# Performance work log

Measured on AMD Instinct MI355X. Metric: run time of the kernel, lower is better.

The kernel has to match this reference:

```python
import jax, jax.numpy as jnp
import numpy as np

BETA = 0.25      # commitment loss weight
DECAY = 0.99     # EMA decay
EPS = 1e-5       # Laplace smoothing for counts


def setup_inputs() -> dict:
    key = jax.random.key(0)
    k1, k2, k3 = jax.random.split(key, 3)
    B, d, h, w, K = 16, 64, 64, 64, 1024
    z_e = jax.random.normal(k1, (B, d, h, w), dtype=jnp.float32)
    codebook = jax.random.normal(k2, (K, d), dtype=jnp.float32)
    ema_count = jnp.ones((K,), dtype=jnp.float32)
    ema_sum = jax.random.normal(k3, (K, d), dtype=jnp.float32)
    return {"z_e": z_e, "codebook": codebook, "ema_count": ema_count, "ema_sum": ema_sum}


def reference(z_e, codebook, ema_count, ema_sum):
    B, d, h, w = z_e.shape
    K = codebook.shape[0]
    # [B,d,h,w] -> [N,d], N = B*h*w
    z_flat = jnp.transpose(z_e, (0, 2, 3, 1)).reshape(-1, d)
    # squared euclidean distances [N,K]
    dist = (jnp.sum(z_flat * z_flat, axis=1, keepdims=True)
            - 2.0 * (z_flat @ codebook.T)
            + jnp.sum(codebook * codebook, axis=1)[None, :])
    indices = jnp.argmin(dist, axis=1)                      # [N] int
    e_k = codebook[indices].reshape(B, h, w, d).transpose(0, 3, 1, 2)  # [B,d,h,w]

    # --- EMA codebook update (training mode, no grad) ---
    zf = jax.lax.stop_gradient(z_flat)
    counts = jax.ops.segment_sum(jnp.ones((zf.shape[0],), dtype=zf.dtype), indices, num_segments=K)
    sums = jax.ops.segment_sum(zf, indices, num_segments=K)
    new_count = ema_count * DECAY + (1.0 - DECAY) * counts
    new_sum = ema_sum * DECAY + (1.0 - DECAY) * sums
    n = jnp.sum(new_count)
    count_s = (new_count + EPS) / (n + K * EPS) * n
    new_codebook = new_sum / count_s[:, None]

    # straight-through estimator
    e_k_ste = z_e + jax.lax.stop_gradient(e_k - z_e)
    L_commit = (jnp.mean((z_e - jax.lax.stop_gradient(e_k)) ** 2)
                + BETA * jnp.mean((jax.lax.stop_gradient(z_e) - e_k) ** 2))
    return (e_k_ste, indices.reshape(B, h, w), L_commit, new_codebook, new_count, new_sum)
```

## Files before the change

kernel.cpp:

```cpp
#include <hip/hip_runtime.h>
#include <hip/hip_bf16.h>
#include <hip/hip_fp16.h>

#define NB 16
#define DD 64
#define HW 4096
#define NTOT 65536
#define KC 1024

#define O_EK   0
#define O_IDX  4194304
#define O_L    4259840
#define O_CB   4259841
#define O_CNT  4325377
#define O_SUM  4326401

#define WS_IDX    0
#define WS_LCPART 65536
#define WS_N      66048
#define WS_CNORM  66560
#define WS_PSUM   67584
#define WS_PCNT   329728
#define WS_FLGC   333824
#define WS_FLGL   334336
#define WS_CBH    399360
#define WS_CBL    432128

#define MARGIN 0.002f
#define MAXFLG 32

typedef _Float16 v8h __attribute__((ext_vector_type(8)));
typedef float    v4f __attribute__((ext_vector_type(4)));

__global__ __launch_bounds__(256) void k_pre(const float* __restrict__ cb,
                                             const float* __restrict__ ema_count,
                                             float* __restrict__ cnorm,
                                             float* __restrict__ n_ws,
                                             unsigned short* __restrict__ cbh,
                                             unsigned short* __restrict__ cbl) {
    const int t = threadIdx.x;
    const int w = (blockIdx.x * 256 + t) >> 6;
    const int l = t & 63;
    float s = 0.f;
    if (l < 16) {
        float4 v = *(const float4*)(cb + (size_t)w * DD + l * 4);
        s = v.x * v.x + v.y * v.y + v.z * v.z + v.w * v.w;
    }
#pragma unroll
    for (int m = 1; m <= 8; m <<= 1) s += __shfl_xor(s, m, 64);
    if (l == 0) cnorm[w] = s;

    const int e4 = blockIdx.x * 256 + t;
    if (e4 < 16384) {
        float4 v4 = ((const float4*)cb)[e4];
        __half hx = __float2half(v4.x), hy = __float2half(v4.y),
               hz = __float2half(v4.z), hw2 = __float2half(v4.w);
        ushort4 h4 = { __half_as_ushort(hx), __half_as_ushort(hy),
                       __half_as_ushort(hz), __half_as_ushort(hw2) };
        ((ushort4*)cbh)[e4] = h4;
        ushort4 l4 = { __half_as_ushort(__float2half(v4.x - __half2float(hx))),
                       __half_as_ushort(__float2half(v4.y - __half2float(hy))),
                       __half_as_ushort(__float2half(v4.z - __half2float(hz))),
                       __half_as_ushort(__float2half(v4.w - __half2float(hw2))) };
        ((ushort4*)cbl)[e4] = l4;
    }

    if (blockIdx.x == 0) {
        __shared__ float red[256];
        red[t] = ema_count[t] + ema_count[t + 256] + ema_count[t + 512] + ema_count[t + 768];
        __syncthreads();
        for (int s2 = 128; s2 >= 1; s2 >>= 1) {
            if (t < s2) red[t] += red[t + s2];
            __syncthreads();
        }
        if (t == 0) n_ws[0] = 0.99f * red[0] + 0.01f * 65536.0f;
    }
}

__global__ __launch_bounds__(256) void k_argmin(const float* __restrict__ z_e,
                                                const unsigned short* __restrict__ cbh,
                                                const unsigned short* __restrict__ cbl,
                                                const float* __restrict__ cnorm,
                                                int* __restrict__ idx_ws,
                                                int* __restrict__ flg_cnt,
                                                int* __restrict__ flg_list,
                                                float* __restrict__ out) {
    __shared__ __align__(16) unsigned short Ah[128 * 72];
    __shared__ __align__(16) unsigned short Al[128 * 72];
    __shared__ __align__(16) unsigned short Bs[2][128 * 72];
    __shared__ __align__(16) float cn_lds[KC];
    __shared__ float znl[128];
    __shared__ int   idx_lds[128];
    __shared__ int   flagrows[128];
    __shared__ int   nflag;

    unsigned short* Bh = &Bs[0][0];
    unsigned short* Bl = &Bs[1][0];
    float* Atf = (float*)&Bs[0][0];

    const int t  = threadIdx.x;
    const int n0 = blockIdx.x * 128;
    const int b   = n0 >> 12;
    const int hw0 = n0 & 4095;
    const float* zbase = z_e + (size_t)b * (DD * HW) + hw0;

    if (t == 0) nflag = 0;
    *(float4*)&cn_lds[t * 4] = *(const float4*)(cnorm + t * 4);

#pragma unroll
    for (int s = 0; s < 8; ++s) {
        int idx = t + s * 256;
        int j   = idx >> 5;
        int i4  = (idx & 31) << 2;
        float4 v = *(const float4*)(zbase + (size_t)j * HW + i4);
        *(float4*)(&Atf[j * 128 + i4]) = v;
    }
    __syncthreads();

    {
        const int m  = t & 127;
        const int j0 = (t >> 7) * 32;
#pragma unroll 4
        for (int jj = 0; jj < 32; jj += 2) {
            int j = j0 + jj;
            float v0 = Atf[j * 128 + m];
            float v1 = Atf[(j + 1) * 128 + m];
            __half h0 = __float2half(v0), h1 = __float2half(v1);
            __half l0 = __float2half(v0 - __half2float(h0));
            __half l1 = __float2half(v1 - __half2float(h1));
            *(unsigned*)&Ah[m * 72 + j] = (unsigned)__half_as_ushort(h0) | ((unsigned)__half_as_ushort(h1) << 16);
            *(unsigned*)&Al[m * 72 + j] = (unsigned)__half_as_ushort(l0) | ((unsigned)__half_as_ushort(l1) << 16);
        }
    }
    __syncthreads();

    if (t < 128) {
        float s = 0.f;
        for (int j = 0; j < 64; ++j) { float a = Atf[j * 128 + t]; s = fmaf(a, a, s); }
        znl[t] = s;
    }

    const int w    = t >> 6;
    const int lane = t & 63;
    const int c    = lane & 15;
    const int q    = lane >> 4;

    v8h Afh[2][2], Afl[2][2];
#pragma unroll
    for (int g = 0; g < 2; ++g) {
        int m = 32 * w + 16 * g + c;
#pragma unroll
        for (int s = 0; s < 2; ++s) {
            Afh[g][s] = *(const v8h*)&Ah[m * 72 + s * 32 + q * 8];
            Afl[g][s] = *(const v8h*)&Al[m * 72 + s * 32 + q * 8];
        }
    }

    float m1v[2][4], m2v[2][4]; int m1i[2][4];
#pragma unroll
    for (int g = 0; g < 2; ++g)
#pragma unroll
        for (int r = 0; r < 4; ++r) { m1v[g][r] = 3.4e38f; m2v[g][r] = 3.4e38f; m1i[g][r] = 0; }

    for (int kt = 0; kt < 8; ++kt) {
        __syncthreads();
#pragma unroll
        for (int s2 = 0; s2 < 4; ++s2) {
            int idx = t + s2 * 256;
            int code = idx >> 3;
            int off  = (idx & 7) * 8;
            size_t gsrc = ((size_t)(kt * 128 + code)) * 64 + off;
            *(uint4*)&Bh[code * 72 + off] = *(const uint4*)(cbh + gsrc);
            *(uint4*)&Bl[code * 72 + off] = *(const uint4*)(cbl + gsrc);
        }
        __syncthreads();

#pragma unroll
        for (int sub = 0; sub < 8; ++sub) {
            const int cl = sub * 16 + c;
            v8h Bfh0 = *(const v8h*)&Bh[cl * 72 + q * 8];
            v8h Bfh1 = *(const v8h*)&Bh[cl * 72 + 32 + q * 8];
            v8h Bfl0 = *(const v8h*)&Bl[cl * 72 + q * 8];
            v8h Bfl1 = *(const v8h*)&Bl[cl * 72 + 32 + q * 8];
            float cnc = cn_lds[kt * 128 + cl];
            const int kg = kt * 128 + cl;
#pragma unroll
            for (int g = 0; g < 2; ++g) {
                v4f acc = {0.f, 0.f, 0.f, 0.f};
                acc = __builtin_amdgcn_mfma_f32_16x16x32_f16(Afh[g][0], Bfh0, acc, 0, 0, 0);
                acc = __builtin_amdgcn_mfma_f32_16x16x32_f16(Afh[g][1], Bfh1, acc, 0, 0, 0);
                acc = __builtin_amdgcn_mfma_f32_16x16x32_f16(Afh[g][0], Bfl0, acc, 0, 0, 0);
                acc = __builtin_amdgcn_mfma_f32_16x16x32_f16(Afh[g][1], Bfl1, acc, 0, 0, 0);
                acc = __builtin_amdgcn_mfma_f32_16x16x32_f16(Afl[g][0], Bfh0, acc, 0, 0, 0);
                acc = __builtin_amdgcn_mfma_f32_16x16x32_f16(Afl[g][1], Bfh1, acc, 0, 0, 0);
#pragma unroll
                for (int r = 0; r < 4; ++r) {
                    float v = fmaf(-2.0f, acc[r], cnc);
                    bool better = v < m1v[g][r];
                    m2v[g][r] = better ? m1v[g][r] : fminf(m2v[g][r], v);
                    m1i[g][r] = better ? kg : m1i[g][r];
                    m1v[g][r] = better ? v : m1v[g][r];
                }
            }
        }
    }

#pragma unroll
    for (int g = 0; g < 2; ++g)
#pragma unroll
        for (int r = 0; r < 4; ++r) {
            float a = m1v[g][r], b2 = m2v[g][r]; int ii = m1i[g][r];
#pragma unroll
            for (int mask = 1; mask <= 8; mask <<= 1) {
                float ov = __shfl_xor(a, mask, 64);
                int   oi = __shfl_xor(ii, mask, 64);
                float o2 = __shfl_xor(b2, mask, 64);
                bool take = (ov < a) || (ov == a && oi < ii);
                float loser = take ? a : ov;
                b2 = fminf(fminf(b2, o2), loser);
                a  = take ? ov : a;
                ii = take ? oi : ii;
            }
            if (c == 0) {
                int row = 32 * w + 16 * g + q * 4 + r;
                idx_lds[row] = ii;
                if ((b2 - a) < MARGIN) { int p = atomicAdd(&nflag, 1); flagrows[p] = row; }
            }
        }
    __syncthreads();

    int nf = nflag; if (nf > MAXFLG) nf = MAXFLG;
    if (t == 0) flg_cnt[blockIdx.x] = nf;
    if (t < nf) flg_list[blockIdx.x * MAXFLG + t] = flagrows[t];

    if (t < 128) {
        int bi = idx_lds[t];
        out[O_IDX + n0 + t] = (float)bi;
        idx_ws[n0 + t] = bi;
    }
}

__global__ __launch_bounds__(256) void k_fix(const float* __restrict__ z_e,
                                             const float* __restrict__ cb,
                                             const float* __restrict__ cnorm,
                                             const int* __restrict__ flg_cnt,
                                             const int* __restrict__ flg_list,
                                             int* __restrict__ idx_ws,
                                             float* __restrict__ out) {
    const int blk = blockIdx.x;
    const int nf = flg_cnt[blk];
    if (nf == 0) return;
    __shared__ float redv4[4];
    __shared__ int   redi4[4];
    const int t = threadIdx.x;
    const int lane = t & 63, w = t >> 6;
    const int n0 = blk * 128;
    const int b   = n0 >> 12;
    const int hw0 = n0 & 4095;

    for (int f = 0; f < nf; ++f) {
        int row = flg_list[blk * MAXFLG + f];
        const float* zrow = z_e + (size_t)b * (DD * HW) + hw0 + row;
        float znr = 0.f;
        for (int j = 0; j < 64; ++j) { float v = zrow[(size_t)j * HW]; znr = fmaf(v, v, znr); }
        float best = 3.4e38f; int bi = 0;
#pragma unroll
        for (int c2 = 0; c2 < 4; ++c2) {
            int k = t * 4 + c2;
            const float* ck = cb + (size_t)k * DD;
            float acc = 0.f;
            for (int j = 0; j < 64; ++j) acc = fmaf(zrow[(size_t)j * HW], ck[j], acc);
            float v = (znr - 2.0f * acc) + cnorm[k];
            if (v < best) { best = v; bi = k; }
        }
#pragma unroll
        for (int mask = 1; mask <= 32; mask <<= 1) {
            float ov = __shfl_xor(best, mask, 64);
            int   oi = __shfl_xor(bi, mask, 64);
            if (ov < best || (ov == best && oi < bi)) { best = ov; bi = oi; }
        }
        if (lane == 0) { redv4[w] = best; redi4[w] = bi; }
        __syncthreads();
        if (t == 0) {
            float bv = redv4[0]; int bix = redi4[0];
#pragma unroll
            for (int w2 = 1; w2 < 4; ++w2)
                if (redv4[w2] < bv || (redv4[w2] == bv && redi4[w2] < bix)) { bv = redv4[w2]; bix = redi4[w2]; }
            idx_ws[n0 + row] = bix;
            out[O_IDX + n0 + row] = (float)bix;
        }
        __syncthreads();
    }
}

__global__ __launch_bounds__(1024) void k_out(const int* __restrict__ idx_ws,
                                              const float* __restrict__ z_e,
                                              const float* __restrict__ cb,
                                              float* __restrict__ psum,
                                              int* __restrict__ pcnt,
                                              float* __restrict__ lc_part,
                                              float* __restrict__ out) {
    __shared__ float acc[KC];
    __shared__ int bins[KC];
    __shared__ float cbj[KC];
    __shared__ float lcr[16];
    const int j = blockIdx.x & 63;
    const int c = blockIdx.x >> 6;
    const int t = threadIdx.x;
    acc[t] = 0.f;
    bins[t] = 0;
    cbj[t] = cb[(size_t)t * DD + j];
    __syncthreads();
    const float* zj = z_e + (size_t)j * HW;
    float* oj = out + O_EK + (size_t)j * HW;
    const int base = c * 16384;
    float lc = 0.f;
#pragma unroll
    for (int i = 0; i < 4; ++i) {
        int n4 = base + i * 4096 + t * 4;
        int b = n4 >> 12, hw = n4 & 4095;
        size_t zoff = (size_t)b * (DD * HW) + hw;
        float4 z4 = *(const float4*)(zj + zoff);
        int4   k4 = *(const int4*)(idx_ws + n4);
        float e0 = cbj[k4.x], e1 = cbj[k4.y], e2 = cbj[k4.z], e3 = cbj[k4.w];
        float4 o4 = { z4.x + (e0 - z4.x), z4.y + (e1 - z4.y),
                      z4.z + (e2 - z4.z), z4.w + (e3 - z4.w) };
        *(float4*)(oj + zoff) = o4;
        float d0 = z4.x - e0, d1 = z4.y - e1, d2 = z4.z - e2, d3 = z4.w - e3;
        lc = fmaf(d0, d0, lc); lc = fmaf(d1, d1, lc);
        lc = fmaf(d2, d2, lc); lc = fmaf(d3, d3, lc);
        atomicAdd(&acc[k4.x], z4.x);
        atomicAdd(&acc[k4.y], z4.y);
        atomicAdd(&acc[k4.z], z4.z);
        atomicAdd(&acc[k4.w], z4.w);
        if (j == 0) {
            atomicAdd(&bins[k4.x], 1); atomicAdd(&bins[k4.y], 1);
            atomicAdd(&bins[k4.z], 1); atomicAdd(&bins[k4.w], 1);
        }
    }
    __syncthreads();
    psum[(size_t)c * 65536 + j * 1024 + t] = acc[t];
    if (j == 0) pcnt[c * 1024 + t] = bins[t];
#pragma unroll
    for (int m = 32; m >= 1; m >>= 1) lc += __shfl_xor(lc, m, 64);
    if ((t & 63) == 0) lcr[t >> 6] = lc;
    __syncthreads();
    if (t == 0) {
        float s = 0.f;
#pragma unroll
        for (int u = 0; u < 16; ++u) s += lcr[u];
        lc_part[blockIdx.x] = s;
    }
}

__global__ __launch_bounds__(1024) void k_epi(const float* __restrict__ psum,
                                              const int* __restrict__ pcnt,
                                              const float* __restrict__ ema_sum,
                                              const float* __restrict__ ema_count,
                                              const float* __restrict__ n_ws,
                                              const float* __restrict__ lc_part,
                                              float* __restrict__ out) {
    const int t = threadIdx.x;
    const int e = blockIdx.x * 1024 + t;
    const int k = e >> 6, j = e & 63;
    float s4 = psum[j * 1024 + k] + psum[65536 + j * 1024 + k]
             + psum[131072 + j * 1024 + k] + psum[196608 + j * 1024 + k];
    float ns = ema_sum[e] * 0.99f + 0.01f * s4;
    out[O_SUM + e] = ns;
    int cnt = pcnt[k] + pcnt[1024 + k] + pcnt[2048 + k] + pcnt[3072 + k];
    float nc = ema_count[k] * 0.99f + 0.01f * (float)cnt;
    float n  = n_ws[0];
    float cs = (nc + 1e-5f) / (n + 1024.0f * 1e-5f) * n;
    out[O_CB + e] = ns / cs;
    if (blockIdx.x == 0) {
        int c2 = pcnt[t] + pcnt[1024 + t] + pcnt[2048 + t] + pcnt[3072 + t];
        out[O_CNT + t] = ema_count[t] * 0.99f + 0.01f * (float)c2;
    }
    if (blockIdx.x == 1) {
        __shared__ float red[512];
        if (t < 512) red[t] = (t < 256) ? lc_part[t] : 0.f;
        __syncthreads();
        for (int s = 256; s >= 1; s >>= 1) {
            if (t < s) red[t] += red[t + s];
            __syncthreads();
        }
        if (t == 0) out[O_L] = 1.25f * red[0] * (1.0f / 4194304.0f);
    }
}

extern "C" void kernel_launch(void* const* d_in, const int* in_sizes, int n_in,
                              void* d_out, int out_size, void* d_ws, size_t ws_size,
                              hipStream_t stream) {
    const float* z_e       = (const float*)d_in[0];
    const float* cb        = (const float*)d_in[1];
    const float* ema_count = (const float*)d_in[2];
    const float* ema_sum   = (const float*)d_in[3];
    float* out             = (float*)d_out;

    float* ws_f      = (float*)d_ws;
    int*   idx_ws    = (int*)d_ws;
    float* lc_part   = ws_f + WS_LCPART;
    float* n_ws      = ws_f + WS_N;
    float* cnorm_ws  = ws_f + WS_CNORM;
    float* psum      = ws_f + WS_PSUM;
    int*   pcnt      = (int*)(ws_f + WS_PCNT);
    int*   flg_cnt   = (int*)(ws_f + WS_FLGC);
    int*   flg_list  = (int*)(ws_f + WS_FLGL);
    unsigned short* cbh = (unsigned short*)(ws_f + WS_CBH);
    unsigned short* cbl = (unsigned short*)(ws_f + WS_CBL);

    k_pre<<<256, 256, 0, stream>>>(cb, ema_count, cnorm_ws, n_ws, cbh, cbl);
    k_argmin<<<NTOT / 128, 256, 0, stream>>>(z_e, cbh, cbl, cnorm_ws, idx_ws, flg_cnt, flg_list, out);
    k_fix<<<NTOT / 128, 256, 0, stream>>>(z_e, cb, cnorm_ws, flg_cnt, flg_list, idx_ws, out);
    k_out<<<256, 1024, 0, stream>>>(idx_ws, z_e, cb, psum, pcnt, lc_part, out);
    k_epi<<<64, 1024, 0, stream>>>(psum, pcnt, ema_sum, ema_count, n_ws, lc_part, out);
}
```

Before: 160.1 us.

## Shrink argmin LDS footprint with chunked layouts and smaller codebook tiles

Replaces the padded row-major LDS tiles with chunk-major [8][rows][8] half layouts, converts z_e in four 16-channel slabs that reuse the B buffer, and halves the codebook tile to 64 codes over 16 iterations. The codebook-norm LDS copy and the unused per-row z-norm computation are removed, and norms are read from global memory instead. The aim is lower shared-memory use per block, allowing more resident blocks, plus conflict-free 16-byte fragment loads. The cost is twice as many barrier-separated tile loads and extra barriers during the slab conversion.

```diff
diff --git a/kernel.cpp b/kernel.cpp
--- a/kernel.cpp
+++ b/kernel.cpp
@@ -85,18 +85,15 @@
                                                 int* __restrict__ flg_cnt,
                                                 int* __restrict__ flg_list,
                                                 float* __restrict__ out) {
-    __shared__ __align__(16) unsigned short Ah[128 * 72];
-    __shared__ __align__(16) unsigned short Al[128 * 72];
-    __shared__ __align__(16) unsigned short Bs[2][128 * 72];
-    __shared__ __align__(16) float cn_lds[KC];
-    __shared__ float znl[128];
-    __shared__ int   idx_lds[128];
-    __shared__ int   flagrows[128];
-    __shared__ int   nflag;
-
-    unsigned short* Bh = &Bs[0][0];
-    unsigned short* Bl = &Bs[1][0];
-    float* Atf = (float*)&Bs[0][0];
+    __shared__ __align__(16) unsigned short A2h[8][128][8];
+    __shared__ __align__(16) unsigned short A2l[8][128][8];
+    __shared__ __align__(16) unsigned short B2h[8][64][8];
+    __shared__ __align__(16) unsigned short B2l[8][64][8];
+    __shared__ int idx_lds[128];
+    __shared__ int flagrows[128];
+    __shared__ int nflag;
+
+    float* slab = (float*)&B2h[0][0][0];
 
     const int t  = threadIdx.x;
     const int n0 = blockIdx.x * 128;
@@ -105,40 +102,40 @@
     const float* zbase = z_e + (size_t)b * (DD * HW) + hw0;
 
     if (t == 0) nflag = 0;
-    *(float4*)&cn_lds[t * 4] = *(const float4*)(cnorm + t * 4);
-
-#pragma unroll
-    for (int s = 0; s < 8; ++s) {
-        int idx = t + s * 256;
-        int j   = idx >> 5;
-        int i4  = (idx & 31) << 2;
-        float4 v = *(const float4*)(zbase + (size_t)j * HW + i4);
-        *(float4*)(&Atf[j * 128 + i4]) = v;
+
+    for (int sl = 0; sl < 4; ++sl) {
+        __syncthreads();
+#pragma unroll
+        for (int s = 0; s < 2; ++s) {
+            int idx = t + s * 256;
+            int j   = idx >> 5;
+            int m4  = (idx & 31) << 2;
+            float4 v = *(const float4*)(zbase + (size_t)(sl * 16 + j) * HW + m4);
+            *(float4*)&slab[j * 128 + m4] = v;
+        }
+        __syncthreads();
+        {
+            const int chl = t >> 7;
+            const int m   = t & 127;
+            const int ch  = sl * 2 + chl;
+            unsigned hv[4], lv[4];
+#pragma unroll
+            for (int p = 0; p < 4; ++p) {
+                float v0 = slab[(chl * 8 + 2 * p    ) * 128 + m];
+                float v1 = slab[(chl * 8 + 2 * p + 1) * 128 + m];
+                __half h0 = __float2half(v0), h1 = __float2half(v1);
+                __half l0 = __float2half(v0 - __half2float(h0));
+                __half l1 = __float2half(v1 - __half2float(h1));
+                hv[p] = (unsigned)__half_as_ushort(h0) | ((unsigned)__half_as_ushort(h1) << 16);
+                lv[p] = (unsigned)__half_as_ushort(l0) | ((unsigned)__half_as_ushort(l1) << 16);
+            }
+            uint4 hq = {hv[0], hv[1], hv[2], hv[3]};
+            uint4 lq = {lv[0], lv[1], lv[2], lv[3]};
+            *(uint4*)&A2h[ch][m][0] = hq;
+            *(uint4*)&A2l[ch][m][0] = lq;
+        }
     }
     __syncthreads();
-
-    {
-        const int m  = t & 127;
-        const int j0 = (t >> 7) * 32;
-#pragma unroll 4
-        for (int jj = 0; jj < 32; jj += 2) {
-            int j = j0 + jj;
-            float v0 = Atf[j * 128 + m];
-            float v1 = Atf[(j + 1) * 128 + m];
-            __half h0 = __float2half(v0), h1 = __float2half(v1);
-            __half l0 = __float2half(v0 - __half2float(h0));
-            __half l1 = __float2half(v1 - __half2float(h1));
-            *(unsigned*)&Ah[m * 72 + j] = (unsigned)__half_as_ushort(h0) | ((unsigned)__half_as_ushort(h1) << 16);
-            *(unsigned*)&Al[m * 72 + j] = (unsigned)__half_as_ushort(l0) | ((unsigned)__half_as_ushort(l1) << 16);
-        }
-    }
-    __syncthreads();
-
-    if (t < 128) {
-        float s = 0.f;
-        for (int j = 0; j < 64; ++j) { float a = Atf[j * 128 + t]; s = fmaf(a, a, s); }
-        znl[t] = s;
-    }
 
     const int w    = t >> 6;
     const int lane = t & 63;
@@ -151,8 +148,8 @@
         int m = 32 * w + 16 * g + c;
 #pragma unroll
         for (int s = 0; s < 2; ++s) {
-            Afh[g][s] = *(const v8h*)&Ah[m * 72 + s * 32 + q * 8];
-            Afl[g][s] = *(const v8h*)&Al[m * 72 + s * 32 + q * 8];
+            Afh[g][s] = *(const v8h*)&A2h[s * 4 + q][m][0];
+            Afl[g][s] = *(const v8h*)&A2l[s * 4 + q][m][0];
         }
     }
 
@@ -162,28 +159,28 @@
 #pragma unroll
         for (int r = 0; r < 4; ++r) { m1v[g][r] = 3.4e38f; m2v[g][r] = 3.4e38f; m1i[g][r] = 0; }
 
-    for (int kt = 0; kt < 8; ++kt) {
-        __syncthreads();
-#pragma unroll
-        for (int s2 = 0; s2 < 4; ++s2) {
-            int idx = t + s2 * 256;
-            int code = idx >> 3;
-            int off  = (idx & 7) * 8;
-            size_t gsrc = ((size_t)(kt * 128 + code)) * 64 + off;
-            *(uint4*)&Bh[code * 72 + off] = *(const uint4*)(cbh + gsrc);
-            *(uint4*)&Bl[code * 72 + off] = *(const uint4*)(cbl + gsrc);
-        }
-        __syncthreads();
-
-#pragma unroll
-        for (int sub = 0; sub < 8; ++sub) {
+    for (int kt = 0; kt < 16; ++kt) {
+        __syncthreads();
+#pragma unroll
+        for (int s2 = 0; s2 < 2; ++s2) {
+            int idx  = t + s2 * 256;
+            int ch   = idx >> 6;
+            int code = idx & 63;
+            size_t gsrc = ((size_t)(kt * 64 + code)) * 64 + ch * 8;
+            *(uint4*)&B2h[ch][code][0] = *(const uint4*)(cbh + gsrc);
+            *(uint4*)&B2l[ch][code][0] = *(const uint4*)(cbl + gsrc);
+        }
+        __syncthreads();
+
+#pragma unroll
+        for (int sub = 0; sub < 4; ++sub) {
             const int cl = sub * 16 + c;
-            v8h Bfh0 = *(const v8h*)&Bh[cl * 72 + q * 8];
-            v8h Bfh1 = *(const v8h*)&Bh[cl * 72 + 32 + q * 8];
-            v8h Bfl0 = *(const v8h*)&Bl[cl * 72 + q * 8];
-            v8h Bfl1 = *(const v8h*)&Bl[cl * 72 + 32 + q * 8];
-            float cnc = cn_lds[kt * 128 + cl];
-            const int kg = kt * 128 + cl;
+            v8h Bfh0 = *(const v8h*)&B2h[q][cl][0];
+            v8h Bfh1 = *(const v8h*)&B2h[4 + q][cl][0];
+            v8h Bfl0 = *(const v8h*)&B2l[q][cl][0];
+            v8h Bfl1 = *(const v8h*)&B2l[4 + q][cl][0];
+            const int kg = kt * 64 + cl;
+            float cnc = cnorm[kg];
 #pragma unroll
             for (int g = 0; g < 2; ++g) {
                 v4f acc = {0.f, 0.f, 0.f, 0.f};
```

Measured after the change: 163.9 us. +2.4%, slower.
